# Kernel tuning notes

Hardware: AMD Instinct MI355X
Metric: run time of the kernel (lower is better)

## Reference

```python
import jax, jax.numpy as jnp
import numpy as np

SIZE = 256        # output distance-map resolution (init arg `size`)
K_SIGN = 100000.0 # tanh sharpness approximating sign() (init arg `k`)
EPS = 1e-05       # smoothing / div-by-zero guard (init arg `eps`)


def setup_inputs() -> dict:
    key = jax.random.key(0)
    # contour (B, N, K, 2) with coordinates in [0, 1]
    contour = jax.random.uniform(key, (2, 4, 64, 2), dtype=jnp.float32)
    return {"contour": contour}


def reference(contour):
    b, n, k, _ = contour.shape
    c = contour.reshape(b * n, 1, k, 2)  # (bn, 1, k, 2)

    ax = jnp.arange(SIZE, dtype=jnp.float32)
    # meshgrid with 'ij' indexing matches torch.meshgrid default
    mesh = jnp.stack(jnp.meshgrid(ax, ax, indexing="ij"), axis=-1).reshape(-1, 2) / SIZE  # (S2, 2)

    diff = c - mesh[None, :, None, :]                      # (bn, S2, k, 2)
    norm_diff = jnp.linalg.norm(diff, axis=-1)             # (bn, S2, k)
    min_diff = jnp.min(norm_diff, axis=2).reshape(b * n, SIZE, SIZE)

    roll_diff = jnp.roll(diff, -1, axis=2)                 # next contour vertex
    # torch: sign = diff * roll(roll_diff, 1, dims=3); sign[...,1]-sign[...,0]
    #      = diff_y * roll_x - diff_x * roll_y  (2D cross product)
    cross = diff[..., 1] * roll_diff[..., 0] - diff[..., 0] * roll_diff[..., 1]
    sign = jnp.tanh(K_SIGN * cross)

    nd = jnp.clip(norm_diff, EPS, None)
    nr = jnp.clip(jnp.linalg.norm(roll_diff, axis=-1), EPS, None)
    dot = jnp.sum(diff * roll_diff, axis=-1)
    angles = jnp.arccos(jnp.clip(dot / (nd * nr), -1.0 + EPS, 1.0 - EPS))

    pi = jnp.arccos(jnp.float32(0.0)) * 2
    sum_angles = jnp.abs(jnp.sum(sign * angles, axis=2) / (2 * pi))  # winding number
    resize = sum_angles.reshape(b * n, SIZE, SIZE)

    prod = resize * min_diff
    dmap = prod / jnp.max(prod)  # global max normalization, as in torch code
    return dmap.reshape(b, n, SIZE, SIZE)
```

## Files before the change

kernel.cpp:

```cpp
#include <hip/hip_runtime.h>
#include <math.h>

#define MS 256
#define KV 64
#define HPX (1.0f / 256.0f)
#define TK 288539.0083f
#define TAUE 1.2e-4f

__global__ __launch_bounds__(256) void cdm_pass1(
    const float* __restrict__ contour,
    float* __restrict__ out,
    float* __restrict__ bmax)
{
    __shared__ __align__(16) float2 vlds[KV + 2];
    __shared__ int   evt[4][MS + 1];
    __shared__ float corr[4][MS];
    __shared__ int   part[4][4];
    __shared__ float wmax[4];

    const int bn = blockIdx.x >> 6;
    const int cq = blockIdx.x & 63;
    const float mx0 = (float)(4 * cq) * HPX;
    const float mx1 = mx0 + HPX;
    const float mx2 = mx0 + 2.0f * HPX;
    const float mx3 = mx0 + 3.0f * HPX;
    const int tid = threadIdx.x;

    for (int i = tid; i < 4 * (MS + 1); i += 256) ((int*)evt)[i] = 0;
    for (int i = tid; i < 4 * MS; i += 256) ((float*)corr)[i] = 0.0f;

    const float2* gsrc = (const float2*)contour + bn * KV;
    if (tid < KV) vlds[tid] = gsrc[tid];
    if (tid == 0) vlds[KV] = gsrc[0];
    __syncthreads();

    {
        const int e = tid & 63;
        const int c = tid >> 6;
        const float mx = mx0 + (float)c * HPX;
        const float2 A = vlds[e];
        const float2 B = vlds[e + 1];
        const float C1 = B.x - A.x;
        const float C0 = fmaf(A.y, B.x, -(A.x * B.y)) + mx * (B.y - A.y);
        const bool  up = B.y > A.y;
        const float lo = fminf(A.y, B.y);
        const float hi = fmaxf(A.y, B.y);
        const float y0 = C0 * __builtin_amdgcn_rcpf(C1);

        const bool cut_low = (up == (C1 > 0.0f));
        const float l = cut_low ? fmaxf(lo, y0) : lo;
        const float h = cut_low ? hi : fminf(hi, y0);
        if (l < h) {
            const int jl = (int)ceilf(fminf(fmaxf(l * 256.0f, 0.0f), 256.0f));
            const int jh = (int)ceilf(fminf(fmaxf(h * 256.0f, 0.0f), 256.0f));
            if (jl < jh) {
                const int dir = up ? 1 : -1;
                atomicAdd(&evt[c][jl], dir);
                atomicAdd(&evt[c][jh], -dir);
            }
        }

        const float aC1 = __builtin_fabsf(C1);
        float wf = TAUE * __builtin_amdgcn_rcpf(aC1) * 256.0f;
        const bool full = !(wf < 300.0f);
        const float y0c = fminf(fmaxf(y0, -4.0f), 4.0f);
        const int W  = (int)fminf(wf, 300.0f) + 1;
        const int jc = (int)(y0c * 256.0f);
        const int sl = (int)ceilf(lo * 256.0f) - 1;
        const int sh = (int)(hi * 256.0f) + 1;
        int j0 = full ? max(sl, 0) : max(max(jc - W, sl), 0);
        int j1 = full ? min(sh, 255) : min(min(jc + W, sh), 255);
        for (int j = j0; j <= j1; ++j) {
            const float my = (float)j * HPX;
            const float cr = fmaf(-my, C1, C0);
            const float acr = __builtin_fabsf(cr);
            if (acr < TAUE) {
                const float dot = fmaf(A.x - mx, B.x - mx, (A.y - my) * (B.y - my));
                if (dot < 0.0f) {
                    const float e2 = __builtin_amdgcn_exp2f(acr * TK);
                    const float d2 = __builtin_amdgcn_rcpf(e2 + 1.0f);
                    atomicAdd(&corr[c][j], __builtin_copysignf(d2, cr));
                }
            }
        }
    }
    __syncthreads();

    int v0 = evt[0][tid];
    int v1 = evt[1][tid];
    int v2 = evt[2][tid];
    int v3 = evt[3][tid];
    const int lane = tid & 63;
    const int wv = tid >> 6;
    #pragma unroll
    for (int off = 1; off < 64; off <<= 1) {
        const int t0 = __shfl_up(v0, off);
        const int t1 = __shfl_up(v1, off);
        const int t2 = __shfl_up(v2, off);
        const int t3 = __shfl_up(v3, off);
        if (lane >= off) { v0 += t0; v1 += t1; v2 += t2; v3 += t3; }
    }
    if (lane == 63) { part[0][wv] = v0; part[1][wv] = v1;
                      part[2][wv] = v2; part[3][wv] = v3; }
    __syncthreads();
    #pragma unroll
    for (int w = 0; w < 3; ++w)
        if (wv > w) { v0 += part[0][w]; v1 += part[1][w];
                      v2 += part[2][w]; v3 += part[3][w]; }

    const float my = (float)tid * HPX;
    float md0 = 1e30f, md1 = 1e30f, md2 = 1e30f, md3 = 1e30f;
    const float4* vp = (const float4*)vlds;
    #pragma unroll 8
    for (int k = 0; k < KV / 2; ++k) {
        const float4 q = vp[k];
        float t, s;
        t = q.y - my; t = t * t;
        s = q.x - mx0; md0 = fminf(md0, fmaf(s, s, t));
        s = q.x - mx1; md1 = fminf(md1, fmaf(s, s, t));
        s = q.x - mx2; md2 = fminf(md2, fmaf(s, s, t));
        s = q.x - mx3; md3 = fminf(md3, fmaf(s, s, t));
        t = q.w - my; t = t * t;
        s = q.z - mx0; md0 = fminf(md0, fmaf(s, s, t));
        s = q.z - mx1; md1 = fminf(md1, fmaf(s, s, t));
        s = q.z - mx2; md2 = fminf(md2, fmaf(s, s, t));
        s = q.z - mx3; md3 = fminf(md3, fmaf(s, s, t));
    }

    const float r0 = __builtin_fabsf((float)v0 + corr[0][tid]);
    const float r1 = __builtin_fabsf((float)v1 + corr[1][tid]);
    const float r2 = __builtin_fabsf((float)v2 + corr[2][tid]);
    const float r3 = __builtin_fabsf((float)v3 + corr[3][tid]);
    const float pv0 = r0 * __builtin_amdgcn_sqrtf(md0);
    const float pv1 = r1 * __builtin_amdgcn_sqrtf(md1);
    const float pv2 = r2 * __builtin_amdgcn_sqrtf(md2);
    const float pv3 = r3 * __builtin_amdgcn_sqrtf(md3);

    float* ob = out + bn * (MS * MS) + (4 * cq) * MS;
    ob[tid] = pv0;
    ob[MS + tid] = pv1;
    ob[2 * MS + tid] = pv2;
    ob[3 * MS + tid] = pv3;

    float m = fmaxf(fmaxf(pv0, pv1), fmaxf(pv2, pv3));
    #pragma unroll
    for (int off = 32; off > 0; off >>= 1)
        m = fmaxf(m, __shfl_xor(m, off));
    if (lane == 0) wmax[wv] = m;
    __syncthreads();
    if (tid == 0)
        bmax[blockIdx.x] = fmaxf(fmaxf(wmax[0], wmax[1]), fmaxf(wmax[2], wmax[3]));
}

__global__ __launch_bounds__(256) void cdm_pass2(
    float4* __restrict__ out, const float* __restrict__ bmax, int nb, int n4)
{
    float m = 0.0f;
    for (int i = threadIdx.x; i < nb; i += 256) m = fmaxf(m, bmax[i]);
    #pragma unroll
    for (int off = 32; off > 0; off >>= 1)
        m = fmaxf(m, __shfl_xor(m, off));

    __shared__ float wm[4];
    if ((threadIdx.x & 63) == 0) wm[threadIdx.x >> 6] = m;
    __syncthreads();
    const float gm  = fmaxf(fmaxf(wm[0], wm[1]), fmaxf(wm[2], wm[3]));
    const float inv = 1.0f / gm;

    const int i = blockIdx.x * 256 + threadIdx.x;
    if (i < n4) {
        float4 v = out[i];
        v.x *= inv; v.y *= inv; v.z *= inv; v.w *= inv;
        out[i] = v;
    }
}

extern "C" void kernel_launch(void* const* d_in, const int* in_sizes, int n_in,
                              void* d_out, int out_size, void* d_ws, size_t ws_size,
                              hipStream_t stream) {
    const float* contour = (const float*)d_in[0];
    float* out  = (float*)d_out;
    float* bmax = (float*)d_ws;

    const int bn = in_sizes[0] / (KV * 2);
    const int npix = bn * MS * MS;

    const int nb = bn * 64;
    cdm_pass1<<<nb, 256, 0, stream>>>(contour, out, bmax);

    const int n4 = npix / 4;
    cdm_pass2<<<(n4 + 255) / 256, 256, 0, stream>>>((float4*)out, bmax, nb, n4);
}
```

Baseline: 16.18 us.

## Fuse max-normalization into main kernel via cooperative grid sync

Merges the two passes into one cooperative kernel. Each block computes its tile, publishes a block max, waits on a grid-wide barrier, reduces all block maxima and writes already-normalized output. This removes the second launch and the re-read and re-write of the whole output map. In exchange it pays for a grid-wide barrier, keeps the tile values live in registers across it, and needs all 512 blocks to be co-resident.

```diff
diff --git a/kernel.cpp b/kernel.cpp
--- a/kernel.cpp
+++ b/kernel.cpp
@@ -1,5 +1,8 @@
 #include <hip/hip_runtime.h>
+#include <hip/hip_cooperative_groups.h>
 #include <math.h>
+
+namespace cg = cooperative_groups;
 
 #define MS 256
 #define KV 64
@@ -7,7 +10,7 @@
 #define TK 288539.0083f
 #define TAUE 1.2e-4f
 
-__global__ __launch_bounds__(256) void cdm_pass1(
+__global__ __launch_bounds__(256) void cdm_fused(
     const float* __restrict__ contour,
     float* __restrict__ out,
     float* __restrict__ bmax)
@@ -136,12 +139,6 @@
     const float pv2 = r2 * __builtin_amdgcn_sqrtf(md2);
     const float pv3 = r3 * __builtin_amdgcn_sqrtf(md3);
 
-    float* ob = out + bn * (MS * MS) + (4 * cq) * MS;
-    ob[tid] = pv0;
-    ob[MS + tid] = pv1;
-    ob[2 * MS + tid] = pv2;
-    ob[3 * MS + tid] = pv3;
-
     float m = fmaxf(fmaxf(pv0, pv1), fmaxf(pv2, pv3));
     #pragma unroll
     for (int off = 32; off > 0; off >>= 1)
@@ -150,29 +147,26 @@
     __syncthreads();
     if (tid == 0)
         bmax[blockIdx.x] = fmaxf(fmaxf(wmax[0], wmax[1]), fmaxf(wmax[2], wmax[3]));
-}
 
-__global__ __launch_bounds__(256) void cdm_pass2(
-    float4* __restrict__ out, const float* __restrict__ bmax, int nb, int n4)
-{
-    float m = 0.0f;
-    for (int i = threadIdx.x; i < nb; i += 256) m = fmaxf(m, bmax[i]);
+    cg::this_grid().sync();
+
+    const int nb = gridDim.x;
+    float g = 0.0f;
+    for (int i = tid; i < nb; i += 256) g = fmaxf(g, bmax[i]);
     #pragma unroll
     for (int off = 32; off > 0; off >>= 1)
-        m = fmaxf(m, __shfl_xor(m, off));
+        g = fmaxf(g, __shfl_xor(g, off));
+    __syncthreads();
+    if (lane == 0) wmax[wv] = g;
+    __syncthreads();
+    const float gm  = fmaxf(fmaxf(wmax[0], wmax[1]), fmaxf(wmax[2], wmax[3]));
+    const float inv = __builtin_amdgcn_rcpf(gm);
 
-    __shared__ float wm[4];
-    if ((threadIdx.x & 63) == 0) wm[threadIdx.x >> 6] = m;
-    __syncthreads();
-    const float gm  = fmaxf(fmaxf(wm[0], wm[1]), fmaxf(wm[2], wm[3]));
-    const float inv = 1.0f / gm;
-
-    const int i = blockIdx.x * 256 + threadIdx.x;
-    if (i < n4) {
-        float4 v = out[i];
-        v.x *= inv; v.y *= inv; v.z *= inv; v.w *= inv;
-        out[i] = v;
-    }
+    float* ob = out + bn * (MS * MS) + (4 * cq) * MS;
+    ob[tid]          = pv0 * inv;
+    ob[MS + tid]     = pv1 * inv;
+    ob[2 * MS + tid] = pv2 * inv;
+    ob[3 * MS + tid] = pv3 * inv;
 }
 
 extern "C" void kernel_launch(void* const* d_in, const int* in_sizes, int n_in,
@@ -183,11 +177,9 @@
     float* bmax = (float*)d_ws;
 
     const int bn = in_sizes[0] / (KV * 2);
-    const int npix = bn * MS * MS;
+    const int nb = bn * 64;
 
-    const int nb = bn * 64;
-    cdm_pass1<<<nb, 256, 0, stream>>>(contour, out, bmax);
-
-    const int n4 = npix / 4;
-    cdm_pass2<<<(n4 + 255) / 256, 256, 0, stream>>>((float4*)out, bmax, nb, n4);
+    void* args[] = { (void*)&contour, (void*)&out, (void*)&bmax };
+    hipLaunchCooperativeKernel((void*)cdm_fused, dim3(nb), dim3(256),
+                               args, 0, stream);
 }
```

Result: slower. 60.16 us (+271.9%).
